# Kernel optimization log

Measured on AMD Instinct MI355X. Metric: run time of the kernel, lower is better.

The kernel has to match this reference:

```python
import jax, jax.numpy as jnp
import numpy as np

B, S, D, E, K = 4, 4096, 2048, 64, 2

def setup_inputs() -> dict:
    key = jax.random.key(0)
    kx, kw = jax.random.split(key)
    x = jax.random.normal(kx, (B, S, D), dtype=jnp.float32)
    W = jax.random.normal(kw, (E, D), dtype=jnp.float32) * (1.0 / np.sqrt(D))
    b = jnp.zeros((E,), dtype=jnp.float32)
    return {"x": x, "W": W, "b": b, "k": K}

def reference(x, W, b, k):
    # logits: [B, S, E]
    logits = jnp.einsum('bsd,ed->bse', x, W) + b
    probs = jax.nn.softmax(logits, axis=-1)
    topk_probs, topk_experts = jax.lax.top_k(probs, k)  # [B,S,k]
    # one-hot over experts, OR-reduce over k -> bool mask [B,S,E]
    onehot = jax.nn.one_hot(topk_experts, E, dtype=jnp.int32)  # [B,S,k,E]
    masks = onehot.sum(axis=-2).astype(jnp.bool_)
    return (masks, probs)
```

## Files before the change

kernel.cpp:

```cpp
#include <hip/hip_runtime.h>
#include <math.h>

#define NTOK    16384
#define DDIM    2048
#define NEXP    64
#define PSTRIDE (NTOK * NEXP)
#define ITERS   32

typedef _Float16 half8   __attribute__((ext_vector_type(8)));
typedef float    floatx4 __attribute__((ext_vector_type(4)));

__global__ __launch_bounds__(256) void wconv_kernel(
    const float* __restrict__ W, _Float16* __restrict__ ws)
{
    const int g    = blockIdx.x * 256 + threadIdx.x;
    const int lane = g & 63;
    const int pl   = (g >> 6) & 1;
    const int j    = (g >> 7) & 3;
    const int i    = (g >> 9) & 31;
    const int h    = (g >> 14) & 1;
    const int e    = j * 16 + (lane & 15);
    const int k    = h * 1024 + i * 32 + (lane >> 4) * 8;

    const float* src = &W[(size_t)e * DDIM + k];
    floatx4 w0 = *(const floatx4*)src;
    floatx4 w1 = *(const floatx4*)(src + 4);

    half8 o;
#pragma unroll
    for (int q = 0; q < 4; ++q) {
        float f0 = w0[q], f1 = w1[q];
        _Float16 h0 = (_Float16)f0, h1 = (_Float16)f1;
        if (pl == 0) { o[q] = h0; o[4 + q] = h1; }
        else {
            o[q]     = (_Float16)((f0 - (float)h0) * 2048.0f);
            o[4 + q] = (_Float16)((f1 - (float)h1) * 2048.0f);
        }
    }
    *(half8*)(ws + (size_t)g * 8) = o;
}

__global__ __launch_bounds__(256, 2) void router_kernel(
    const float* __restrict__ x,
    const _Float16* __restrict__ ws,
    const float* __restrict__ bias,
    float* __restrict__ out)
{
    __shared__ float rbuf[2048];

    const int tid  = threadIdx.x;
    const int lane = tid & 63;
    const int wid  = tid >> 6;
    const int t    = wid >> 1;
    const int h    = wid & 1;
    const int t0   = blockIdx.x * 32 + t * 16;
    const int mrow = lane & 15;
    const int quad = lane >> 4;

    floatx4 acc_hh[4], acc_md[4];
#pragma unroll
    for (int j = 0; j < 4; ++j) { acc_hh[j] = (floatx4)0.0f; acc_md[j] = (floatx4)0.0f; }

    const float* xrow = x + (size_t)(t0 + mrow) * DDIM + h * 1024 + quad * 8;
    const _Float16* wbase = ws + (size_t)h * 131072 + (size_t)lane * 8;

    floatx4 xs0[ITERS], xs1[ITERS];
    half8   bsh[ITERS][4], bsl[ITERS][4];

#pragma unroll
    for (int i = 0; i < 2; ++i) {
        xs0[i] = *(const floatx4*)(xrow + i * 32);
        xs1[i] = *(const floatx4*)(xrow + i * 32 + 4);
    }
#pragma unroll
    for (int j = 0; j < 4; ++j) {
        bsh[0][j] = *(const half8*)(wbase + (size_t)(j * 2    ) * 512);
        bsl[0][j] = *(const half8*)(wbase + (size_t)(j * 2 + 1) * 512);
    }

#pragma unroll
    for (int i = 0; i < ITERS; ++i) {
        if (i + 2 < ITERS) {
            xs0[i + 2] = *(const floatx4*)(xrow + (i + 2) * 32);
            xs1[i + 2] = *(const floatx4*)(xrow + (i + 2) * 32 + 4);
        }
        if (i + 1 < ITERS) {
            const _Float16* gb = wbase + (size_t)(i + 1) * 4096;
#pragma unroll
            for (int j = 0; j < 4; ++j) {
                bsh[i + 1][j] = *(const half8*)(gb + (size_t)(j * 2    ) * 512);
                bsl[i + 1][j] = *(const half8*)(gb + (size_t)(j * 2 + 1) * 512);
            }
        }

        half8 a_hi, a_lo;
#pragma unroll
        for (int q = 0; q < 4; ++q) {
            float fv = xs0[i][q];
            _Float16 hh = (_Float16)fv;
            a_hi[q] = hh;
            a_lo[q] = (_Float16)((fv - (float)hh) * 2048.0f);
        }
#pragma unroll
        for (int q = 0; q < 4; ++q) {
            float fv = xs1[i][q];
            _Float16 hh = (_Float16)fv;
            a_hi[4 + q] = hh;
            a_lo[4 + q] = (_Float16)((fv - (float)hh) * 2048.0f);
        }

#pragma unroll
        for (int j = 0; j < 4; ++j) {
            acc_hh[j] = __builtin_amdgcn_mfma_f32_16x16x32_f16(a_hi, bsh[i][j], acc_hh[j], 0, 0, 0);
            acc_md[j] = __builtin_amdgcn_mfma_f32_16x16x32_f16(a_hi, bsl[i][j], acc_md[j], 0, 0, 0);
            acc_md[j] = __builtin_amdgcn_mfma_f32_16x16x32_f16(a_lo, bsh[i][j], acc_md[j], 0, 0, 0);
        }
    }

    float lg[4][4];
#pragma unroll
    for (int j = 0; j < 4; ++j)
#pragma unroll
        for (int r = 0; r < 4; ++r)
            lg[j][r] = acc_hh[j][r] + acc_md[j][r] * (1.0f / 2048.0f);

    __syncthreads();
    if (h == 1) {
#pragma unroll
        for (int j = 0; j < 4; ++j)
#pragma unroll
            for (int r = 0; r < 4; ++r)
                rbuf[t * 1024 + (j * 4 + r) * 64 + lane] = lg[j][r];
    }
    __syncthreads();
    if (h == 1) return;

#pragma unroll
    for (int j = 0; j < 4; ++j) {
        const float bj = bias[j * 16 + mrow];
#pragma unroll
        for (int r = 0; r < 4; ++r)
            lg[j][r] += rbuf[t * 1024 + (j * 4 + r) * 64 + lane] + bj;
    }

    const int c = mrow;
#pragma unroll
    for (int r = 0; r < 4; ++r) {
        const int trow = t0 + quad * 4 + r;

        float m = lg[0][r];
#pragma unroll
        for (int j = 1; j < 4; ++j) m = fmaxf(m, lg[j][r]);
#pragma unroll
        for (int off = 1; off <= 8; off <<= 1) m = fmaxf(m, __shfl_xor(m, off));

        float pj[4], s = 0.0f;
#pragma unroll
        for (int j = 0; j < 4; ++j) { pj[j] = __expf(lg[j][r] - m); s += pj[j]; }
#pragma unroll
        for (int off = 1; off <= 8; off <<= 1) s += __shfl_xor(s, off);
        const float rinv = 1.0f / s;

        float v1 = -1e30f, v2 = -1e30f; int i1 = -1, i2 = -1;
#pragma unroll
        for (int j = 0; j < 4; ++j) {
            float v = lg[j][r]; int e = j * 16 + c;
            if (v > v1 || (v == v1 && e < i1)) { v2 = v1; i2 = i1; v1 = v; i1 = e; }
            else if (v > v2 || (v == v2 && e < i2)) { v2 = v; i2 = e; }
        }
#pragma unroll
        for (int off = 1; off <= 8; off <<= 1) {
            float u1 = __shfl_xor(v1, off); int q1 = __shfl_xor(i1, off);
            float u2 = __shfl_xor(v2, off); int q2 = __shfl_xor(i2, off);
            if (u1 > v1 || (u1 == v1 && q1 < i1)) {
                if (v1 > u2 || (v1 == u2 && i1 < q2)) { v2 = v1; i2 = i1; }
                else                                   { v2 = u2; i2 = q2; }
                v1 = u1; i1 = q1;
            } else {
                if (u1 > v2 || (u1 == v2 && q1 < i2)) { v2 = u1; i2 = q1; }
            }
        }

#pragma unroll
        for (int j = 0; j < 4; ++j) {
            const int col = j * 16 + c;
            const size_t o = (size_t)trow * NEXP + col;
            out[o]           = (col == i1 || col == i2) ? 1.0f : 0.0f;
            out[PSTRIDE + o] = pj[j] * rinv;
        }
    }
}

extern "C" void kernel_launch(void* const* d_in, const int* in_sizes, int n_in,
                              void* d_out, int out_size, void* d_ws, size_t ws_size,
                              hipStream_t stream) {
    const float* x = (const float*)d_in[0];
    const float* W = (const float*)d_in[1];
    const float* b = (const float*)d_in[2];
    (void)in_sizes; (void)n_in; (void)out_size; (void)ws_size;
    float* out = (float*)d_out;

    _Float16* ws = (_Float16*)d_ws;

    hipLaunchKernelGGL(wconv_kernel, dim3(128), dim3(256), 0, stream, W, ws);
    hipLaunchKernelGGL(router_kernel, dim3(NTOK / 32), dim3(256), 0, stream, x, ws, b, out);
}
```

Baseline: 248.5 us.

## Split-K GEMM with LDS-staged weights via async global_load_lds and separate reduce epilogue

Replaces the single router kernel with a split-K GEMM: each 512-thread block handles 256 tokens over a quarter of D. The pre-split fp16 weights are staged into double-buffered LDS with global_load_lds DMA so the eight waves share them, and x is prefetched one step ahead in registers. Partial logits go to a workspace buffer, and a second kernel sums the four partials, adds bias, and runs softmax and top-2. The aim is to cut redundant per-wave weight fetches and the huge register-unrolled prefetch arrays. In exchange it adds a partial-sum round trip through global memory and an extra launch.

Result: faster. 209.6 us (-15.6%).

```diff
diff --git a/kernel.cpp b/kernel.cpp
--- a/kernel.cpp
+++ b/kernel.cpp
@@ -5,7 +5,9 @@
 #define DDIM    2048
 #define NEXP    64
 #define PSTRIDE (NTOK * NEXP)
-#define ITERS   32
+
+#define AS1 __attribute__((address_space(1)))
+#define AS3 __attribute__((address_space(3)))
 
 typedef _Float16 half8   __attribute__((ext_vector_type(8)));
 typedef float    floatx4 __attribute__((ext_vector_type(4)));
@@ -13,14 +15,14 @@
 __global__ __launch_bounds__(256) void wconv_kernel(
     const float* __restrict__ W, _Float16* __restrict__ ws)
 {
-    const int g    = blockIdx.x * 256 + threadIdx.x;
-    const int lane = g & 63;
-    const int pl   = (g >> 6) & 1;
-    const int j    = (g >> 7) & 3;
-    const int i    = (g >> 9) & 31;
-    const int h    = (g >> 14) & 1;
-    const int e    = j * 16 + (lane & 15);
-    const int k    = h * 1024 + i * 32 + (lane >> 4) * 8;
+    const int g  = blockIdx.x * 256 + threadIdx.x;
+    const int s  = g >> 10;
+    const int c  = g & 1023;
+    const int q  = c & 3;
+    const int e  = (c >> 2) & 63;
+    const int pl = (c >> 8) & 1;
+    const int kk = (c >> 9) & 1;
+    const int k  = s * 64 + kk * 32 + q * 8;
 
     const float* src = &W[(size_t)e * DDIM + k];
     floatx4 w0 = *(const floatx4*)src;
@@ -28,135 +30,180 @@
 
     half8 o;
 #pragma unroll
-    for (int q = 0; q < 4; ++q) {
-        float f0 = w0[q], f1 = w1[q];
+    for (int i = 0; i < 4; ++i) {
+        float f0 = w0[i], f1 = w1[i];
         _Float16 h0 = (_Float16)f0, h1 = (_Float16)f1;
-        if (pl == 0) { o[q] = h0; o[4 + q] = h1; }
+        if (pl == 0) { o[i] = h0; o[4 + i] = h1; }
         else {
-            o[q]     = (_Float16)((f0 - (float)h0) * 2048.0f);
-            o[4 + q] = (_Float16)((f1 - (float)h1) * 2048.0f);
+            o[i]     = (_Float16)((f0 - (float)h0) * 2048.0f);
+            o[4 + i] = (_Float16)((f1 - (float)h1) * 2048.0f);
         }
     }
     *(half8*)(ws + (size_t)g * 8) = o;
 }
 
-__global__ __launch_bounds__(256, 2) void router_kernel(
+__global__ __launch_bounds__(512, 2) void gemm_partial(
     const float* __restrict__ x,
     const _Float16* __restrict__ ws,
+    float* __restrict__ part)
+{
+    __shared__ __align__(16) char lds[2][16384];
+
+    const int tid  = threadIdx.x;
+    const int lane = tid & 63;
+    const int wid  = tid >> 6;
+    const int bm   = blockIdx.x >> 2;
+    const int ks   = blockIdx.x & 3;
+    const int T0   = bm * 256;
+    const int mrow = lane & 15;
+    const int quad = lane >> 4;
+
+    floatx4 acc_hh[2][4], acc_md[2][4];
+#pragma unroll
+    for (int m = 0; m < 2; ++m)
+#pragma unroll
+        for (int j = 0; j < 4; ++j) { acc_hh[m][j] = (floatx4)0.0f; acc_md[m][j] = (floatx4)0.0f; }
+
+    const float* xbase = x + (size_t)(T0 + wid * 32 + mrow) * DDIM + ks * 512 + quad * 8;
+    const char* wsrc = (const char*)ws + (size_t)(ks * 8) * 16384 + (size_t)lane * 16;
+
+#define DMA(P, B)                                                              \
+    {                                                                          \
+        const char* gs = wsrc + (size_t)(P) * 16384;                           \
+        __builtin_amdgcn_global_load_lds(                                      \
+            (const AS1 unsigned int*)(const void*)(gs + wid * 1024),           \
+            (AS3 unsigned int*)(void*)&lds[B][wid * 1024], 16, 0, 0);          \
+        __builtin_amdgcn_global_load_lds(                                      \
+            (const AS1 unsigned int*)(const void*)(gs + 8192 + wid * 1024),    \
+            (AS3 unsigned int*)(void*)&lds[B][8192 + wid * 1024], 16, 0, 0);   \
+    }
+
+#define XLOAD(P, DST)                                                          \
+    {                                                                          \
+        _Pragma("unroll")                                                      \
+        for (int m_ = 0; m_ < 2; ++m_)                                         \
+        _Pragma("unroll")                                                      \
+        for (int kk_ = 0; kk_ < 2; ++kk_)                                      \
+        _Pragma("unroll")                                                      \
+        for (int hf_ = 0; hf_ < 2; ++hf_)                                      \
+            (DST)[m_ * 4 + kk_ * 2 + hf_] = *(const floatx4*)(                 \
+                xbase + (size_t)m_ * 16 * DDIM + (P) * 64 + kk_ * 32 + hf_ * 4); \
+    }
+
+    floatx4 xc[8], xn[8];
+
+    XLOAD(0, xc);
+    DMA(0, 0);
+    __syncthreads();
+
+    for (int p = 0; p < 8; ++p) {
+        if (p < 7) {
+            XLOAD(p + 1, xn);
+            DMA(p + 1, (p + 1) & 1);
+        }
+
+        const _Float16* lb = (const _Float16*)lds[p & 1];
+#pragma unroll
+        for (int kk = 0; kk < 2; ++kk) {
+            half8 bh[4], bl[4];
+#pragma unroll
+            for (int j = 0; j < 4; ++j) {
+                const int e = j * 16 + mrow;
+                bh[j] = *(const half8*)(lb + ((kk * 2 + 0) * 64 + e) * 32 + quad * 8);
+                bl[j] = *(const half8*)(lb + ((kk * 2 + 1) * 64 + e) * 32 + quad * 8);
+            }
+#pragma unroll
+            for (int m = 0; m < 2; ++m) {
+                half8 a_hi, a_lo;
+                floatx4 v0 = xc[m * 4 + kk * 2];
+                floatx4 v1 = xc[m * 4 + kk * 2 + 1];
+#pragma unroll
+                for (int q = 0; q < 4; ++q) {
+                    float fv = v0[q];
+                    _Float16 hh = (_Float16)fv;
+                    a_hi[q] = hh;
+                    a_lo[q] = (_Float16)((fv - (float)hh) * 2048.0f);
+                }
+#pragma unroll
+                for (int q = 0; q < 4; ++q) {
+                    float fv = v1[q];
+                    _Float16 hh = (_Float16)fv;
+                    a_hi[4 + q] = hh;
+                    a_lo[4 + q] = (_Float16)((fv - (float)hh) * 2048.0f);
+                }
+#pragma unroll
+                for (int j = 0; j < 4; ++j) {
+                    acc_hh[m][j] = __builtin_amdgcn_mfma_f32_16x16x32_f16(a_hi, bh[j], acc_hh[m][j], 0, 0, 0);
+                    acc_md[m][j] = __builtin_amdgcn_mfma_f32_16x16x32_f16(a_hi, bl[j], acc_md[m][j], 0, 0, 0);
+                    acc_md[m][j] = __builtin_amdgcn_mfma_f32_16x16x32_f16(a_lo, bh[j], acc_md[m][j], 0, 0, 0);
+                }
+            }
+        }
+
+        if (p < 7) {
+#pragma unroll
+            for (int i = 0; i < 8; ++i) xc[i] = xn[i];
+        }
+        __syncthreads();
+    }
+
+    float* pw = part + ((size_t)(ks * 64 + bm)) * 16384 + wid * 2048 + lane;
+#pragma unroll
+    for (int m = 0; m < 2; ++m)
+#pragma unroll
+        for (int j = 0; j < 4; ++j)
+#pragma unroll
+            for (int r = 0; r < 4; ++r)
+                pw[m * 1024 + (j * 4 + r) * 64] =
+                    acc_hh[m][j][r] + acc_md[m][j][r] * (1.0f / 2048.0f);
+}
+
+__global__ __launch_bounds__(256) void reduce_epilogue(
+    const float* __restrict__ part,
     const float* __restrict__ bias,
     float* __restrict__ out)
 {
-    __shared__ float rbuf[2048];
-
     const int tid  = threadIdx.x;
     const int lane = tid & 63;
-    const int wid  = tid >> 6;
-    const int t    = wid >> 1;
-    const int h    = wid & 1;
-    const int t0   = blockIdx.x * 32 + t * 16;
+    const int u    = blockIdx.x * 4 + (tid >> 6);
+    const int bm   = u >> 4;
+    const int w8   = (u >> 1) & 7;
+    const int m    = u & 1;
     const int mrow = lane & 15;
     const int quad = lane >> 4;
-
-    floatx4 acc_hh[4], acc_md[4];
-#pragma unroll
-    for (int j = 0; j < 4; ++j) { acc_hh[j] = (floatx4)0.0f; acc_md[j] = (floatx4)0.0f; }
-
-    const float* xrow = x + (size_t)(t0 + mrow) * DDIM + h * 1024 + quad * 8;
-    const _Float16* wbase = ws + (size_t)h * 131072 + (size_t)lane * 8;
-
-    floatx4 xs0[ITERS], xs1[ITERS];
-    half8   bsh[ITERS][4], bsl[ITERS][4];
-
-#pragma unroll
-    for (int i = 0; i < 2; ++i) {
-        xs0[i] = *(const floatx4*)(xrow + i * 32);
-        xs1[i] = *(const floatx4*)(xrow + i * 32 + 4);
-    }
-#pragma unroll
-    for (int j = 0; j < 4; ++j) {
-        bsh[0][j] = *(const half8*)(wbase + (size_t)(j * 2    ) * 512);
-        bsl[0][j] = *(const half8*)(wbase + (size_t)(j * 2 + 1) * 512);
-    }
-
-#pragma unroll
-    for (int i = 0; i < ITERS; ++i) {
-        if (i + 2 < ITERS) {
-            xs0[i + 2] = *(const floatx4*)(xrow + (i + 2) * 32);
-            xs1[i + 2] = *(const floatx4*)(xrow + (i + 2) * 32 + 4);
-        }
-        if (i + 1 < ITERS) {
-            const _Float16* gb = wbase + (size_t)(i + 1) * 4096;
-#pragma unroll
-            for (int j = 0; j < 4; ++j) {
-                bsh[i + 1][j] = *(const half8*)(gb + (size_t)(j * 2    ) * 512);
-                bsl[i + 1][j] = *(const half8*)(gb + (size_t)(j * 2 + 1) * 512);
-            }
-        }
-
-        half8 a_hi, a_lo;
-#pragma unroll
-        for (int q = 0; q < 4; ++q) {
-            float fv = xs0[i][q];
-            _Float16 hh = (_Float16)fv;
-            a_hi[q] = hh;
-            a_lo[q] = (_Float16)((fv - (float)hh) * 2048.0f);
-        }
-#pragma unroll
-        for (int q = 0; q < 4; ++q) {
-            float fv = xs1[i][q];
-            _Float16 hh = (_Float16)fv;
-            a_hi[4 + q] = hh;
-            a_lo[4 + q] = (_Float16)((fv - (float)hh) * 2048.0f);
-        }
-
-#pragma unroll
-        for (int j = 0; j < 4; ++j) {
-            acc_hh[j] = __builtin_amdgcn_mfma_f32_16x16x32_f16(a_hi, bsh[i][j], acc_hh[j], 0, 0, 0);
-            acc_md[j] = __builtin_amdgcn_mfma_f32_16x16x32_f16(a_hi, bsl[i][j], acc_md[j], 0, 0, 0);
-            acc_md[j] = __builtin_amdgcn_mfma_f32_16x16x32_f16(a_lo, bsh[i][j], acc_md[j], 0, 0, 0);
-        }
-    }
+    const int tb   = bm * 256 + w8 * 32 + m * 16;
+
+    const float* pb = part + (size_t)bm * 16384 + w8 * 2048 + m * 1024 + lane;
 
     float lg[4][4];
-#pragma unroll
-    for (int j = 0; j < 4; ++j)
-#pragma unroll
-        for (int r = 0; r < 4; ++r)
-            lg[j][r] = acc_hh[j][r] + acc_md[j][r] * (1.0f / 2048.0f);
-
-    __syncthreads();
-    if (h == 1) {
-#pragma unroll
-        for (int j = 0; j < 4; ++j)
-#pragma unroll
-            for (int r = 0; r < 4; ++r)
-                rbuf[t * 1024 + (j * 4 + r) * 64 + lane] = lg[j][r];
-    }
-    __syncthreads();
-    if (h == 1) return;
-
 #pragma unroll
     for (int j = 0; j < 4; ++j) {
         const float bj = bias[j * 16 + mrow];
 #pragma unroll
-        for (int r = 0; r < 4; ++r)
-            lg[j][r] += rbuf[t * 1024 + (j * 4 + r) * 64 + lane] + bj;
+        for (int r = 0; r < 4; ++r) {
+            const int f = j * 4 + r;
+            float s0 = pb[(size_t)0 * 1048576 + f * 64];
+            float s1 = pb[(size_t)1 * 1048576 + f * 64];
+            float s2 = pb[(size_t)2 * 1048576 + f * 64];
+            float s3 = pb[(size_t)3 * 1048576 + f * 64];
+            lg[j][r] = (s0 + s1) + (s2 + s3) + bj;
+        }
     }
 
     const int c = mrow;
 #pragma unroll
     for (int r = 0; r < 4; ++r) {
-        const int trow = t0 + quad * 4 + r;
-
-        float m = lg[0][r];
-#pragma unroll
-        for (int j = 1; j < 4; ++j) m = fmaxf(m, lg[j][r]);
-#pragma unroll
-        for (int off = 1; off <= 8; off <<= 1) m = fmaxf(m, __shfl_xor(m, off));
+        const int trow = tb + quad * 4 + r;
+
+        float mx = lg[0][r];
+#pragma unroll
+        for (int j = 1; j < 4; ++j) mx = fmaxf(mx, lg[j][r]);
+#pragma unroll
+        for (int off = 1; off <= 8; off <<= 1) mx = fmaxf(mx, __shfl_xor(mx, off));
 
         float pj[4], s = 0.0f;
 #pragma unroll
-        for (int j = 0; j < 4; ++j) { pj[j] = __expf(lg[j][r] - m); s += pj[j]; }
+        for (int j = 0; j < 4; ++j) { pj[j] = __expf(lg[j][r] - mx); s += pj[j]; }
 #pragma unroll
         for (int off = 1; off <= 8; off <<= 1) s += __shfl_xor(s, off);
         const float rinv = 1.0f / s;
@@ -200,8 +247,10 @@
     (void)in_sizes; (void)n_in; (void)out_size; (void)ws_size;
     float* out = (float*)d_out;
 
-    _Float16* ws = (_Float16*)d_ws;
-
-    hipLaunchKernelGGL(wconv_kernel, dim3(128), dim3(256), 0, stream, W, ws);
-    hipLaunchKernelGGL(router_kernel, dim3(NTOK / 32), dim3(256), 0, stream, x, ws, b, out);
-}
+    _Float16* ws  = (_Float16*)d_ws;
+    float*    prt = (float*)((char*)d_ws + (1 << 19));
+
+    hipLaunchKernelGGL(wconv_kernel,    dim3(128), dim3(256), 0, stream, W, ws);
+    hipLaunchKernelGGL(gemm_partial,    dim3(256), dim3(512), 0, stream, x, ws, prt);
+    hipLaunchKernelGGL(reduce_epilogue, dim3(256), dim3(256), 0, stream, prt, b, out);
+}
```
